# Kernel optimization log

Measured on AMD Instinct MI355X. Metric: run time of the kernel, lower is better.

The kernel has to match this reference:

```python
import jax, jax.numpy as jnp
import numpy as np

EMBED_DIM = 1024
NUM_HEADS = 16
HEAD_DIM = EMBED_DIM // NUM_HEADS
B, T_Q, T_K = 2, 2048, 2048


def setup_inputs() -> dict:
    key = jax.random.key(0)
    ks = jax.random.split(key, 11)
    s = 1.0 / np.sqrt(EMBED_DIM)
    return {
        "query": jax.random.normal(ks[0], (B, T_Q, EMBED_DIM), jnp.float32),
        "key": jax.random.normal(ks[1], (B, T_K, EMBED_DIM), jnp.float32),
        "value": jax.random.normal(ks[2], (B, T_K, EMBED_DIM), jnp.float32),
        "Wq": jax.random.normal(ks[3], (EMBED_DIM, EMBED_DIM), jnp.float32) * s,
        "bq": jnp.zeros((EMBED_DIM,), jnp.float32),
        "Wk": jax.random.normal(ks[4], (EMBED_DIM, EMBED_DIM), jnp.float32) * s,
        "bk": jnp.zeros((EMBED_DIM,), jnp.float32),
        "Wv": jax.random.normal(ks[5], (EMBED_DIM, EMBED_DIM), jnp.float32) * s,
        "bv": jnp.zeros((EMBED_DIM,), jnp.float32),
        "Wo": jax.random.normal(ks[6], (EMBED_DIM, EMBED_DIM), jnp.float32) * s,
        "bo": jnp.zeros((EMBED_DIM,), jnp.float32),
    }


def reference(query, key, value, Wq, bq, Wk, bk, Wv, bv, Wo, bo):
    b, tq, _ = query.shape
    tk = key.shape[1]
    # projections -> [B, H, T, Dh]
    q = (query @ Wq.T + bq).reshape(b, tq, NUM_HEADS, HEAD_DIM).transpose(0, 2, 1, 3)
    k = (key @ Wk.T + bk).reshape(b, tk, NUM_HEADS, HEAD_DIM).transpose(0, 2, 1, 3)
    v = (value @ Wv.T + bv).reshape(b, tk, NUM_HEADS, HEAD_DIM).transpose(0, 2, 1, 3)
    scores = jnp.einsum("bhqd,bhkd->bhqk", q, k) / np.sqrt(HEAD_DIM)
    attn = jax.nn.softmax(scores, axis=-1)
    attn = jnp.nan_to_num(attn, nan=0.0)  # matches torch.nan_to_num; dropout is eval-mode identity
    out = jnp.einsum("bhqk,bhkd->bhqd", attn, v)
    out = out.transpose(0, 2, 1, 3).reshape(b, tq, EMBED_DIM)
    return out @ Wo.T + bo
```

## Files before the change

### kernel.cpp

```cpp
#include <hip/hip_runtime.h>
#include <hip/hip_bf16.h>
#include <cmath>


typedef short bf16x8 __attribute__((ext_vector_type(8)));
typedef short bf16x4 __attribute__((ext_vector_type(4)));
typedef float f32x4 __attribute__((ext_vector_type(4)));

#define B_ 2
#define T_ 2048
#define E_ 1024
#define H_ 16
#define DH_ 64
#define M_ 4096
#define QSCALE 0.1803368801111204f

static __device__ __forceinline__ short f2bf(float f) {
    __hip_bfloat16 h = __float2bfloat16(f);
    return *reinterpret_cast<short*>(&h);
}

static __device__ __forceinline__ float bf2f(short s) {
    unsigned u = ((unsigned)(unsigned short)s) << 16;
    float f;
    __builtin_memcpy(&f, &u, 4);
    return f;
}

static __device__ __forceinline__ short f2bf_r(float f) {
    unsigned u;
    __builtin_memcpy(&u, &f, 4);
    return (short)((u + 0x8000u) >> 16);
}

static __device__ __forceinline__ float fast_exp2(float x) {
#if __has_builtin(__builtin_amdgcn_exp2f)
    return __builtin_amdgcn_exp2f(x);
#else
    float y;
    asm volatile("v_exp_f32 %0, %1" : "=v"(y) : "v"(x));
    return y;
#endif
}

static __device__ __forceinline__ bf16x8 cvt8(const float4 a, const float4 b) {
    bf16x8 r;
    r[0] = f2bf(a.x); r[1] = f2bf(a.y); r[2] = f2bf(a.z); r[3] = f2bf(a.w);
    r[4] = f2bf(b.x); r[5] = f2bf(b.y); r[6] = f2bf(b.z); r[7] = f2bf(b.w);
    return r;
}

static __device__ __forceinline__ void async_copy16(const short* g, short* l) {
    __builtin_amdgcn_global_load_lds(
        (const __attribute__((address_space(1))) unsigned int*)g,
        (__attribute__((address_space(3))) unsigned int*)l, 16, 0, 0);
}

__global__ __launch_bounds__(256) void conv_bf16(
    const float* __restrict__ q, const float* __restrict__ k, const float* __restrict__ v,
    const float* __restrict__ wq, const float* __restrict__ wk,
    const float* __restrict__ wv, const float* __restrict__ wo,
    short* __restrict__ qo, short* __restrict__ ko, short* __restrict__ vo,
    short* __restrict__ wqo, short* __restrict__ wko,
    short* __restrict__ wvo, short* __restrict__ woo) {
    const int y = blockIdx.y;
    const float* src; short* dst; int n;
    switch (y) {
        case 0: src = q;  dst = qo;  n = M_ * E_; break;
        case 1: src = k;  dst = ko;  n = M_ * E_; break;
        case 2: src = v;  dst = vo;  n = M_ * E_; break;
        case 3: src = wq; dst = wqo; n = E_ * E_; break;
        case 4: src = wk; dst = wko; n = E_ * E_; break;
        case 5: src = wv; dst = wvo; n = E_ * E_; break;
        default: src = wo; dst = woo; n = E_ * E_; break;
    }
    const int idx = (blockIdx.x * 256 + threadIdx.x) * 8;
    if (idx >= n) return;
    const float4* p = (const float4*)(src + idx);
    *(bf16x8*)(dst + idx) = cvt8(p[0], p[1]);
}

template <int CMODE>
__device__ __forceinline__ void gemm128_tile(const short* __restrict__ A,
                                             const short* __restrict__ W,
                                             const float* __restrict__ bias,
                                             void* __restrict__ C, int bx, int by,
                                             float scale) {
    __shared__ short Asm[128 * 64];
    __shared__ short Wsm[128 * 64];
    const int tid = threadIdx.x;
    const int wave = tid >> 6, lane = tid & 63, quad = lane >> 4, l16 = lane & 15;
    const int wr = wave >> 1, wc = wave & 1;
    const int m_base = by * 128, n_base = bx * 128;
    const int xk = l16 & 7;
    const int srowA = (lane >> 3), scc = lane & 7;

    f32x4 acc[4][4] = {};

    for (int k0 = 0; k0 < E_; k0 += 64) {
#pragma unroll
        for (int i = 0; i < 4; i++) {
            const int row = i * 32 + wave * 8 + srowA;
            const int gc = (scc ^ (row & 7)) * 8;
            async_copy16(&A[(size_t)(m_base + row) * E_ + k0 + gc],
                         &Asm[(i * 256 + wave * 64) * 8]);
            async_copy16(&W[(size_t)(n_base + row) * E_ + k0 + gc],
                         &Wsm[(i * 256 + wave * 64) * 8]);
        }
        __syncthreads();

#pragma unroll
        for (int ks = 0; ks < 2; ks++) {
            bf16x8 af[4], wf[4];
#pragma unroll
            for (int i = 0; i < 4; i++) {
                const int rw = wr * 64 + i * 16 + l16;
                af[i] = *(const bf16x8*)&Asm[rw * 64 + (((ks * 4 + quad) ^ xk) * 8)];
            }
#pragma unroll
            for (int j = 0; j < 4; j++) {
                const int rw = wc * 64 + j * 16 + l16;
                wf[j] = *(const bf16x8*)&Wsm[rw * 64 + (((ks * 4 + quad) ^ xk) * 8)];
            }
#pragma unroll
            for (int i = 0; i < 4; i++)
#pragma unroll
                for (int j = 0; j < 4; j++)
                    acc[i][j] = __builtin_amdgcn_mfma_f32_16x16x32_bf16(af[i], wf[j], acc[i][j], 0, 0, 0);
        }
        __syncthreads();
    }

    if (CMODE == 2) {
#pragma unroll
        for (int j = 0; j < 4; j++) {
            const int col = n_base + wc * 64 + j * 16 + l16;
            const float bval = bias[col];
            const int h = col >> 6, d = col & 63;
#pragma unroll
            for (int i = 0; i < 4; i++) {
                const int m0 = m_base + wr * 64 + i * 16 + quad * 4;
                const int b = m0 >> 11, t0 = m0 & 2047;
                bf16x4 v;
#pragma unroll
                for (int r = 0; r < 4; r++) v[r] = f2bf(acc[i][j][r] + bval);
                *(bf16x4*)&((short*)C)[((size_t)(b * H_ + h) * DH_ + d) * T_ + t0] = v;
            }
        }
    } else {
#pragma unroll
        for (int j = 0; j < 4; j++) {
            const int col = n_base + wc * 64 + j * 16 + l16;
            const float bval = bias[col];
#pragma unroll
            for (int i = 0; i < 4; i++)
#pragma unroll
                for (int r = 0; r < 4; r++) {
                    const int m = m_base + wr * 64 + i * 16 + quad * 4 + r;
                    ((short*)C)[(size_t)m * E_ + col] = f2bf((acc[i][j][r] + bval) * scale);
                }
        }
    }
}

__global__ __launch_bounds__(256) void qkv_gemm_fast(
    const short* __restrict__ q, const short* __restrict__ k, const short* __restrict__ v,
    const short* __restrict__ Wq, const short* __restrict__ Wk, const short* __restrict__ Wv,
    const float* __restrict__ bq, const float* __restrict__ bk, const float* __restrict__ bv,
    short* __restrict__ Qb, short* __restrict__ Kb, short* __restrict__ Vtb) {
    const int z = blockIdx.z;
    if (z == 0)      gemm128_tile<0>(q, Wq, bq, Qb,  blockIdx.x, blockIdx.y, QSCALE);
    else if (z == 1) gemm128_tile<0>(k, Wk, bk, Kb,  blockIdx.x, blockIdx.y, 1.0f);
    else             gemm128_tile<2>(v, Wv, bv, Vtb, blockIdx.x, blockIdx.y, 1.0f);
}

__global__ __launch_bounds__(256) void o_gemm_fast(const short* __restrict__ A,
                                                   const short* __restrict__ W,
                                                   const float* __restrict__ bias,
                                                   float* __restrict__ C) {
    __shared__ short Asm[128 * 64];
    __shared__ short Wsm[64 * 64];
    const int tid = threadIdx.x;
    const int wave = tid >> 6, lane = tid & 63, quad = lane >> 4, l16 = lane & 15;
    const int m_base = blockIdx.y * 128, n_base = blockIdx.x * 64;
    const int xk = l16 & 7;
    const int srowA = (lane >> 3), scc = lane & 7;

    f32x4 acc[2][4] = {};

    for (int k0 = 0; k0 < E_; k0 += 64) {
#pragma unroll
        for (int i = 0; i < 4; i++) {
            const int row = i * 32 + wave * 8 + srowA;
            const int gc = (scc ^ (row & 7)) * 8;
            async_copy16(&A[(size_t)(m_base + row) * E_ + k0 + gc],
                         &Asm[(i * 256 + wave * 64) * 8]);
        }
#pragma unroll
        for (int i = 0; i < 2; i++) {
            const int row = i * 32 + wave * 8 + srowA;
            const int gc = (scc ^ (row & 7)) * 8;
            async_copy16(&W[(size_t)(n_base + row) * E_ + k0 + gc],
                         &Wsm[(i * 256 + wave * 64) * 8]);
        }
        __syncthreads();

#pragma unroll
        for (int ks = 0; ks < 2; ks++) {
            bf16x8 af[2], wf[4];
#pragma unroll
            for (int i = 0; i < 2; i++) {
                const int rw = wave * 32 + i * 16 + l16;
                af[i] = *(const bf16x8*)&Asm[rw * 64 + (((ks * 4 + quad) ^ xk) * 8)];
            }
#pragma unroll
            for (int j = 0; j < 4; j++) {
                const int rw = j * 16 + l16;
                wf[j] = *(const bf16x8*)&Wsm[rw * 64 + (((ks * 4 + quad) ^ xk) * 8)];
            }
#pragma unroll
            for (int i = 0; i < 2; i++)
#pragma unroll
                for (int j = 0; j < 4; j++)
                    acc[i][j] = __builtin_amdgcn_mfma_f32_16x16x32_bf16(af[i], wf[j], acc[i][j], 0, 0, 0);
        }
        __syncthreads();
    }

#pragma unroll
    for (int j = 0; j < 4; j++) {
        const int col = n_base + j * 16 + l16;
        const float bval = bias[col];
#pragma unroll
        for (int i = 0; i < 2; i++)
#pragma unroll
            for (int r = 0; r < 4; r++) {
                const int m = m_base + wave * 32 + i * 16 + quad * 4 + r;
                C[(size_t)m * E_ + col] = acc[i][j][r] + bval;
            }
    }
}

__global__ __launch_bounds__(256) void attn_split(const short* __restrict__ Qb,
                                                  const short* __restrict__ Kb,
                                                  const short* __restrict__ Vtb,
                                                  short* __restrict__ Op,
                                                  float* __restrict__ Ls) {
    __shared__ short Kl[2][64][68];
    __shared__ short Vl[2][64][68];
    __shared__ short Pl[4][32][68];

    const int tid = threadIdx.x;
    const int wave = tid >> 6, lane = tid & 63, quad = lane >> 4, l16 = lane & 15;
    const int bh = blockIdx.x;
    const int b = bh >> 4, h = bh & 15;
    const int ksp = blockIdx.z;
    const int q0 = blockIdx.y * 128 + wave * 32;
    const int kt0 = ksp * (T_ / 2);
    const size_t base = ((size_t)b * T_) * E_ + (size_t)h * DH_;
    const size_t vbase = (size_t)bh * DH_ * T_;
    short* Opk = Op + (size_t)ksp * M_ * E_;
    float* Lsk = Ls + (size_t)ksp * 32 * T_ + (size_t)bh * T_;

    bf16x8 qf[2][2];
#pragma unroll
    for (int rt = 0; rt < 2; rt++)
#pragma unroll
        for (int ks = 0; ks < 2; ks++)
            qf[rt][ks] = *(const bf16x8*)&Qb[base + (size_t)(q0 + rt * 16 + l16) * E_ + ks * 32 + quad * 8];

    bf16x8 ones;
#pragma unroll
    for (int j = 0; j < 8; j++) ones[j] = (short)0x3F80;

    f32x4 oacc[2][4] = {};
    f32x4 lacc[2] = {};

    const int srow = tid >> 2;
    const int sc = (tid & 3) * 16;

    {
        const size_t krow = base + (size_t)(kt0 + srow) * E_;
        *(bf16x8*)&Kl[0][srow][sc]     = *(const bf16x8*)&Kb[krow + sc];
        *(bf16x8*)&Kl[0][srow][sc + 8] = *(const bf16x8*)&Kb[krow + sc + 8];
        const size_t vrow = vbase + (size_t)srow * T_ + kt0;
        *(bf16x8*)&Vl[0][srow][sc]     = *(const bf16x8*)&Vtb[vrow + sc];
        *(bf16x8*)&Vl[0][srow][sc + 8] = *(const bf16x8*)&Vtb[vrow + sc + 8];
    }
    __syncthreads();

    for (int it = 0; it < T_ / 128; it++) {
        const int cur = it & 1;
        const bool have = (it + 1) < T_ / 128;

        bf16x8 nk0, nk1, nv0, nv1;
        if (have) {
            const int kt = kt0 + (it + 1) * 64;
            const size_t krow = base + (size_t)(kt + srow) * E_;
            nk0 = *(const bf16x8*)&Kb[krow + sc];
            nk1 = *(const bf16x8*)&Kb[krow + sc + 8];
            const size_t vrow = vbase + (size_t)srow * T_ + kt;
            nv0 = *(const bf16x8*)&Vtb[vrow + sc];
            nv1 = *(const bf16x8*)&Vtb[vrow + sc + 8];
        }

        f32x4 sacc[2][4] = {};
#pragma unroll
        for (int ks = 0; ks < 2; ks++) {
            bf16x8 kf[4];
#pragma unroll
            for (int kn = 0; kn < 4; kn++)
                kf[kn] = *(const bf16x8*)&Kl[cur][kn * 16 + l16][ks * 32 + quad * 8];
#pragma unroll
            for (int rt = 0; rt < 2; rt++)
#pragma unroll
                for (int kn = 0; kn < 4; kn++)
                    sacc[rt][kn] = __builtin_amdgcn_mfma_f32_16x16x32_bf16(qf[rt][ks], kf[kn], sacc[rt][kn], 0, 0, 0);
        }

#pragma unroll
        for (int rt = 0; rt < 2; rt++)
#pragma unroll
            for (int r = 0; r < 4; r++) {
                short* prow = &Pl[wave][rt * 16 + quad * 4 + r][0];
                prow[l16]      = f2bf_r(fast_exp2(sacc[rt][0][r]));
                prow[16 + l16] = f2bf_r(fast_exp2(sacc[rt][1][r]));
                prow[32 + l16] = f2bf_r(fast_exp2(sacc[rt][2][r]));
                prow[48 + l16] = f2bf_r(fast_exp2(sacc[rt][3][r]));
            }
        asm volatile("s_waitcnt lgkmcnt(0)" ::: "memory");

#pragma unroll
        for (int ks = 0; ks < 2; ks++) {
            bf16x8 pf[2];
#pragma unroll
            for (int rt = 0; rt < 2; rt++)
                pf[rt] = *(const bf16x8*)&Pl[wave][rt * 16 + l16][ks * 32 + quad * 8];
#pragma unroll
            for (int rt = 0; rt < 2; rt++)
                lacc[rt] = __builtin_amdgcn_mfma_f32_16x16x32_bf16(pf[rt], ones, lacc[rt], 0, 0, 0);
#pragma unroll
            for (int dn = 0; dn < 4; dn++) {
                bf16x8 vf = *(const bf16x8*)&Vl[cur][dn * 16 + l16][ks * 32 + quad * 8];
#pragma unroll
                for (int rt = 0; rt < 2; rt++)
                    oacc[rt][dn] = __builtin_amdgcn_mfma_f32_16x16x32_bf16(pf[rt], vf, oacc[rt][dn], 0, 0, 0);
            }
        }

        if (have) {
            *(bf16x8*)&Kl[cur ^ 1][srow][sc]     = nk0;
            *(bf16x8*)&Kl[cur ^ 1][srow][sc + 8] = nk1;
            *(bf16x8*)&Vl[cur ^ 1][srow][sc]     = nv0;
            *(bf16x8*)&Vl[cur ^ 1][srow][sc + 8] = nv1;
        }
        __syncthreads();
    }

#pragma unroll
    for (int rt = 0; rt < 2; rt++) {
#pragma unroll
        for (int dn = 0; dn < 4; dn++)
#pragma unroll
            for (int r = 0; r < 4; r++)
                Opk[base + (size_t)(q0 + rt * 16 + quad * 4 + r) * E_ + dn * 16 + l16] =
                    f2bf(oacc[rt][dn][r]);
        if (l16 == 0) {
#pragma unroll
            for (int r = 0; r < 4; r++)
                Lsk[q0 + rt * 16 + quad * 4 + r] = lacc[rt][r];
        }
    }
}

__global__ __launch_bounds__(256) void combine(const short* __restrict__ Op,
                                               const float* __restrict__ Ls,
                                               short* __restrict__ Qb) {
    const int idx = (blockIdx.x * 256 + threadIdx.x) * 8;
    const int row = idx >> 10;
    const int e = idx & 1023;
    const int h = e >> 6;
    const int b = row >> 11, t = row & 2047;
    const size_t lidx = ((size_t)(b * H_ + h)) * T_ + t;
    const float l = Ls[lidx] + Ls[(size_t)32 * T_ + lidx];
    const float inv = 1.0f / l;
    bf16x8 a = *(const bf16x8*)&Op[idx];
    bf16x8 c = *(const bf16x8*)&Op[(size_t)M_ * E_ + idx];
    bf16x8 o;
#pragma unroll
    for (int j = 0; j < 8; j++) o[j] = f2bf((bf2f(a[j]) + bf2f(c[j])) * inv);
    *(bf16x8*)&Qb[idx] = o;
}

__global__ __launch_bounds__(256) void attn(short* __restrict__ QO,
                                            const short* __restrict__ Kb,
                                            const short* __restrict__ Vtb) {
    __shared__ short Kl[2][64][68];
    __shared__ short Vl[2][64][68];
    __shared__ short Pl[4][32][68];

    const int tid = threadIdx.x;
    const int wave = tid >> 6, lane = tid & 63, quad = lane >> 4, l16 = lane & 15;
    const int bh = blockIdx.x;
    const int b = bh >> 4, h = bh & 15;
    const int q0 = blockIdx.y * 128 + wave * 32;
    const size_t base = ((size_t)b * T_) * E_ + (size_t)h * DH_;
    const size_t vbase = (size_t)bh * DH_ * T_;

    bf16x8 qf[2][2];
#pragma unroll
    for (int rt = 0; rt < 2; rt++)
#pragma unroll
        for (int ks = 0; ks < 2; ks++)
            qf[rt][ks] = *(const bf16x8*)&QO[base + (size_t)(q0 + rt * 16 + l16) * E_ + ks * 32 + quad * 8];

    bf16x8 ones;
#pragma unroll
    for (int j = 0; j < 8; j++) ones[j] = (short)0x3F80;

    f32x4 oacc[2][4] = {};
    f32x4 lacc[2] = {};

    const int srow = tid >> 2;
    const int sc = (tid & 3) * 16;

    {
        const size_t krow = base + (size_t)srow * E_;
        *(bf16x8*)&Kl[0][srow][sc]     = *(const bf16x8*)&Kb[krow + sc];
        *(bf16x8*)&Kl[0][srow][sc + 8] = *(const bf16x8*)&Kb[krow + sc + 8];
        const size_t vrow = vbase + (size_t)srow * T_;
        *(bf16x8*)&Vl[0][srow][sc]     = *(const bf16x8*)&Vtb[vrow + sc];
        *(bf16x8*)&Vl[0][srow][sc + 8] = *(const bf16x8*)&Vtb[vrow + sc + 8];
    }
    __syncthreads();

    for (int it = 0; it < T_ / 64; it++) {
        const int cur = it & 1;
        const bool have = (it + 1) < T_ / 64;

        bf16x8 nk0, nk1, nv0, nv1;
        if (have) {
            const int kt = (it + 1) * 64;
            const size_t krow = base + (size_t)(kt + srow) * E_;
            nk0 = *(const bf16x8*)&Kb[krow + sc];
            nk1 = *(const bf16x8*)&Kb[krow + sc + 8];
            const size_t vrow = vbase + (size_t)srow * T_ + kt;
            nv0 = *(const bf16x8*)&Vtb[vrow + sc];
            nv1 = *(const bf16x8*)&Vtb[vrow + sc + 8];
        }

        f32x4 sacc[2][4] = {};
#pragma unroll
        for (int ks = 0; ks < 2; ks++) {
            bf16x8 kf[4];
#pragma unroll
            for (int kn = 0; kn < 4; kn++)
                kf[kn] = *(const bf16x8*)&Kl[cur][kn * 16 + l16][ks * 32 + quad * 8];
#pragma unroll
            for (int rt = 0; rt < 2; rt++)
#pragma unroll
                for (int kn = 0; kn < 4; kn++)
                    sacc[rt][kn] = __builtin_amdgcn_mfma_f32_16x16x32_bf16(qf[rt][ks], kf[kn], sacc[rt][kn], 0, 0, 0);
        }

#pragma unroll
        for (int rt = 0; rt < 2; rt++)
#pragma unroll
            for (int r = 0; r < 4; r++) {
                short* prow = &Pl[wave][rt * 16 + quad * 4 + r][0];
                prow[l16]      = f2bf_r(fast_exp2(sacc[rt][0][r]));
                prow[16 + l16] = f2bf_r(fast_exp2(sacc[rt][1][r]));
                prow[32 + l16] = f2bf_r(fast_exp2(sacc[rt][2][r]));
                prow[48 + l16] = f2bf_r(fast_exp2(sacc[rt][3][r]));
            }
        asm volatile("s_waitcnt lgkmcnt(0)" ::: "memory");

#pragma unroll
        for (int ks = 0; ks < 2; ks++) {
            bf16x8 pf[2];
#pragma unroll
            for (int rt = 0; rt < 2; rt++)
                pf[rt] = *(const bf16x8*)&Pl[wave][rt * 16 + l16][ks * 32 + quad * 8];
#pragma unroll
            for (int rt = 0; rt < 2; rt++)
                lacc[rt] = __builtin_amdgcn_mfma_f32_16x16x32_bf16(pf[rt], ones, lacc[rt], 0, 0, 0);
#pragma unroll
            for (int dn = 0; dn < 4; dn++) {
                bf16x8 vf = *(const bf16x8*)&Vl[cur][dn * 16 + l16][ks * 32 + quad * 8];
#pragma unroll
                for (int rt = 0; rt < 2; rt++)
                    oacc[rt][dn] = __builtin_amdgcn_mfma_f32_16x16x32_bf16(pf[rt], vf, oacc[rt][dn], 0, 0, 0);
            }
        }

        if (have) {
            *(bf16x8*)&Kl[cur ^ 1][srow][sc]     = nk0;
            *(bf16x8*)&Kl[cur ^ 1][srow][sc + 8] = nk1;
            *(bf16x8*)&Vl[cur ^ 1][srow][sc]     = nv0;
            *(bf16x8*)&Vl[cur ^ 1][srow][sc + 8] = nv1;
        }
        __syncthreads();
    }

    float inv[2][4];
#pragma unroll
    for (int rt = 0; rt < 2; rt++)
#pragma unroll
        for (int r = 0; r < 4; r++) inv[rt][r] = 1.0f / lacc[rt][r];

#pragma unroll
    for (int rt = 0; rt < 2; rt++)
#pragma unroll
        for (int dn = 0; dn < 4; dn++)
#pragma unroll
            for (int r = 0; r < 4; r++) {
                const float v = oacc[rt][dn][r] * inv[rt][r];
                QO[base + (size_t)(q0 + rt * 16 + quad * 4 + r) * E_ + dn * 16 + l16] = f2bf(v);
            }
}

template <int A_BF16, int CMODE>
__device__ __forceinline__ void gemm_tile(const void* __restrict__ A,
                                          const float* __restrict__ W,
                                          const float* __restrict__ bias,
                                          void* __restrict__ C, int bx, int by,
                                          float scale) {
    __shared__ short Alds[128][40];
    __shared__ short Wlds[128][40];
    const int tid = threadIdx.x;
    const int wave = tid >> 6, lane = tid & 63, quad = lane >> 4, l16 = lane & 15;
    const int wr = wave >> 1, wc = wave & 1;
    const int m_base = by * 128, n_base = bx * 128;
    const int srow = tid >> 1, sch = (tid & 1) * 16;

    f32x4 acc[4][4] = {};

    for (int k0 = 0; k0 < E_; k0 += 32) {
        bf16x8 av0, av1, wv0, wv1;
        if (A_BF16) {
            const short* Ab = (const short*)A;
            av0 = *(const bf16x8*)&Ab[(size_t)(m_base + srow) * E_ + k0 + sch];
            av1 = *(const bf16x8*)&Ab[(size_t)(m_base + srow) * E_ + k0 + sch + 8];
        } else {
            const float4* p = (const float4*)((const float*)A +
                              (size_t)(m_base + srow) * E_ + k0 + sch);
            av0 = cvt8(p[0], p[1]);
            av1 = cvt8(p[2], p[3]);
        }
        {
            const float4* p = (const float4*)(W + (size_t)(n_base + srow) * E_ + k0 + sch);
            wv0 = cvt8(p[0], p[1]);
            wv1 = cvt8(p[2], p[3]);
        }
        *(bf16x8*)&Alds[srow][sch]     = av0;
        *(bf16x8*)&Alds[srow][sch + 8] = av1;
        *(bf16x8*)&Wlds[srow][sch]     = wv0;
        *(bf16x8*)&Wlds[srow][sch + 8] = wv1;
        __syncthreads();

        bf16x8 af[4], bfv[4];
#pragma unroll
        for (int i = 0; i < 4; i++)
            af[i] = *(const bf16x8*)&Alds[wr * 64 + i * 16 + l16][quad * 8];
#pragma unroll
        for (int j = 0; j < 4; j++)
            bfv[j] = *(const bf16x8*)&Wlds[wc * 64 + j * 16 + l16][quad * 8];
#pragma unroll
        for (int i = 0; i < 4; i++)
#pragma unroll
            for (int j = 0; j < 4; j++)
                acc[i][j] = __builtin_amdgcn_mfma_f32_16x16x32_bf16(af[i], bfv[j], acc[i][j], 0, 0, 0);
        __syncthreads();
    }

    if (CMODE == 2) {
#pragma unroll
        for (int j = 0; j < 4; j++) {
            const int col = n_base + wc * 64 + j * 16 + l16;
            const float bval = bias[col];
            const int h = col >> 6, d = col & 63;
#pragma unroll
            for (int i = 0; i < 4; i++) {
                const int m0 = m_base + wr * 64 + i * 16 + quad * 4;
                const int b = m0 >> 11, t0 = m0 & 2047;
                bf16x4 v;
#pragma unroll
                for (int r = 0; r < 4; r++) v[r] = f2bf(acc[i][j][r] + bval);
                *(bf16x4*)&((short*)C)[((size_t)(b * H_ + h) * DH_ + d) * T_ + t0] = v;
            }
        }
    } else {
#pragma unroll
        for (int j = 0; j < 4; j++) {
            const int col = n_base + wc * 64 + j * 16 + l16;
            const float bval = bias[col];
#pragma unroll
            for (int i = 0; i < 4; i++)
#pragma unroll
                for (int r = 0; r < 4; r++) {
                    const int m = m_base + wr * 64 + i * 16 + quad * 4 + r;
                    const float v = (acc[i][j][r] + bval) * scale;
                    if (CMODE == 1) ((float*)C)[(size_t)m * E_ + col] = v;
                    else            ((short*)C)[(size_t)m * E_ + col] = f2bf(v);
                }
        }
    }
}

__global__ __launch_bounds__(256) void qkv_gemm_slow(
    const float* __restrict__ q, const float* __restrict__ k, const float* __restrict__ v,
    const float* __restrict__ Wq, const float* __restrict__ Wk, const float* __restrict__ Wv,
    const float* __restrict__ bq, const float* __restrict__ bk, const float* __restrict__ bv,
    short* __restrict__ Qb, short* __restrict__ Kb, short* __restrict__ Vtb) {
    const int z = blockIdx.z;
    if (z == 0)      gemm_tile<0, 0>(q, Wq, bq, Qb,  blockIdx.x, blockIdx.y, QSCALE);
    else if (z == 1) gemm_tile<0, 0>(k, Wk, bk, Kb,  blockIdx.x, blockIdx.y, 1.0f);
    else             gemm_tile<0, 2>(v, Wv, bv, Vtb, blockIdx.x, blockIdx.y, 1.0f);
}

__global__ __launch_bounds__(256) void o_gemm_slow(const short* __restrict__ A,
                                                   const float* __restrict__ W,
                                                   const float* __restrict__ bias,
                                                   float* __restrict__ C) {
    gemm_tile<1, 1>(A, W, bias, C, blockIdx.x, blockIdx.y, 1.0f);
}

extern "C" void kernel_launch(void* const* d_in, const int* in_sizes, int n_in,
                              void* d_out, int out_size, void* d_ws, size_t ws_size,
                              hipStream_t stream) {
    const float* query = (const float*)d_in[0];
    const float* key   = (const float*)d_in[1];
    const float* value = (const float*)d_in[2];
    const float* Wq = (const float*)d_in[3];
    const float* bq = (const float*)d_in[4];
    const float* Wk = (const float*)d_in[5];
    const float* bk = (const float*)d_in[6];
    const float* Wv = (const float*)d_in[7];
    const float* bv = (const float*)d_in[8];
    const float* Wo = (const float*)d_in[9];
    const float* bo = (const float*)d_in[10];

    const size_t NE = (size_t)M_ * E_;
    const size_t WE = (size_t)E_ * E_;

    short* Qb  = (short*)d_ws;
    short* Vtb = Qb + NE;
    short* Kb  = (short*)d_out;

    dim3 blk(256);
    const bool fast = ws_size >= (size_t)48 * 1024 * 1024;

    if (fast) {
        short* Qin = Vtb + NE;
        short* Kin = Qin + NE;
        short* Vin = Kin + NE;
        short* Wqb = Vin + NE;
        short* Wkb = Wqb + WE;
        short* Wvb = Wkb + WE;
        short* Wob = Wvb + WE;

        conv_bf16<<<dim3(2048, 7), blk, 0, stream>>>(query, key, value, Wq, Wk, Wv, Wo,
                                                     Qin, Kin, Vin, Wqb, Wkb, Wvb, Wob);
        qkv_gemm_fast<<<dim3(8, 32, 3), blk, 0, stream>>>(Qin, Kin, Vin,
                                                          Wqb, Wkb, Wvb, bq, bk, bv,
                                                          Qb, Kb, Vtb);
        attn_split<<<dim3(B_ * H_, T_ / 128, 2), blk, 0, stream>>>(
            Qb, Kb, Vtb, Qin, (float*)Vin);
        combine<<<dim3((M_ * E_) / (256 * 8)), blk, 0, stream>>>(
            Qin, (const float*)Vin, Qb);
        o_gemm_fast<<<dim3(16, 32), blk, 0, stream>>>(Qb, Wob, bo, (float*)d_out);
    } else {
        qkv_gemm_slow<<<dim3(8, 32, 3), blk, 0, stream>>>(query, key, value,
                                                          Wq, Wk, Wv, bq, bk, bv,
                                                          Qb, Kb, Vtb);
        attn<<<dim3(B_ * H_, T_ / 128), blk, 0, stream>>>(Qb, Kb, Vtb);
        o_gemm_slow<<<dim3(8, 32), blk, 0, stream>>>(Qb, Wo, bo, (float*)d_out);
    }
}
```

Baseline: 245.4 us.

## Enlarge attention query tile, use async swizzled K/V loads, stage V-transpose stores

Result: faster. 235.4 us (-4.0%).

```diff
diff --git a/kernel.cpp b/kernel.cpp
--- a/kernel.cpp
+++ b/kernel.cpp
@@ -86,8 +86,9 @@
                                              const float* __restrict__ bias,
                                              void* __restrict__ C, int bx, int by,
                                              float scale) {
-    __shared__ short Asm[128 * 64];
-    __shared__ short Wsm[128 * 64];
+    __shared__ short SMEM[128 * 132];
+    short* Asm = SMEM;
+    short* Wsm = SMEM + 128 * 64;
     const int tid = threadIdx.x;
     const int wave = tid >> 6, lane = tid & 63, quad = lane >> 4, l16 = lane & 15;
     const int wr = wave >> 1, wc = wave & 1;
@@ -134,18 +135,27 @@
     if (CMODE == 2) {
 #pragma unroll
         for (int j = 0; j < 4; j++) {
-            const int col = n_base + wc * 64 + j * 16 + l16;
-            const float bval = bias[col];
-            const int h = col >> 6, d = col & 63;
+            const int drow = wc * 64 + j * 16 + l16;
+            const float bval = bias[n_base + drow];
 #pragma unroll
             for (int i = 0; i < 4; i++) {
-                const int m0 = m_base + wr * 64 + i * 16 + quad * 4;
-                const int b = m0 >> 11, t0 = m0 & 2047;
+                const int tcol = wr * 64 + i * 16 + quad * 4;
                 bf16x4 v;
 #pragma unroll
                 for (int r = 0; r < 4; r++) v[r] = f2bf(acc[i][j][r] + bval);
-                *(bf16x4*)&((short*)C)[((size_t)(b * H_ + h) * DH_ + d) * T_ + t0] = v;
-            }
+                *(bf16x4*)&SMEM[drow * 132 + tcol] = v;
+            }
+        }
+        __syncthreads();
+        const int bb = m_base >> 11, t0 = m_base & 2047;
+#pragma unroll
+        for (int u0 = 0; u0 < 8; u0++) {
+            const int u = u0 * 256 + tid;
+            const int row = u >> 4, ch = u & 15;
+            const int col = n_base + row;
+            const int hh = col >> 6, dd = col & 63;
+            bf16x8 val = *(const bf16x8*)&SMEM[row * 132 + ch * 8];
+            *(bf16x8*)&((short*)C)[((size_t)(bb * H_ + hh) * DH_ + dd) * T_ + t0 + ch * 8] = val;
         }
     } else {
 #pragma unroll
@@ -241,13 +251,13 @@
     }
 }
 
-__global__ __launch_bounds__(256) void attn_split(const short* __restrict__ Qb,
-                                                  const short* __restrict__ Kb,
-                                                  const short* __restrict__ Vtb,
-                                                  short* __restrict__ Op,
-                                                  float* __restrict__ Ls) {
-    __shared__ short Kl[2][64][68];
-    __shared__ short Vl[2][64][68];
+__global__ __launch_bounds__(256, 2) void attn_split(const short* __restrict__ Qb,
+                                                     const short* __restrict__ Kb,
+                                                     const short* __restrict__ Vtb,
+                                                     short* __restrict__ Op,
+                                                     float* __restrict__ Ls) {
+    __shared__ short Kl[2][64 * 64];
+    __shared__ short Vl[2][64 * 64];
     __shared__ short Pl[4][32][68];
 
     const int tid = threadIdx.x;
@@ -255,16 +265,16 @@
     const int bh = blockIdx.x;
     const int b = bh >> 4, h = bh & 15;
     const int ksp = blockIdx.z;
-    const int q0 = blockIdx.y * 128 + wave * 32;
+    const int q0 = blockIdx.y * 256 + wave * 64;
     const int kt0 = ksp * (T_ / 2);
     const size_t base = ((size_t)b * T_) * E_ + (size_t)h * DH_;
     const size_t vbase = (size_t)bh * DH_ * T_;
     short* Opk = Op + (size_t)ksp * M_ * E_;
     float* Lsk = Ls + (size_t)ksp * 32 * T_ + (size_t)bh * T_;
 
-    bf16x8 qf[2][2];
-#pragma unroll
-    for (int rt = 0; rt < 2; rt++)
+    bf16x8 qf[4][2];
+#pragma unroll
+    for (int rt = 0; rt < 4; rt++)
 #pragma unroll
         for (int ks = 0; ks < 2; ks++)
             qf[rt][ks] = *(const bf16x8*)&Qb[base + (size_t)(q0 + rt * 16 + l16) * E_ + ks * 32 + quad * 8];
@@ -273,103 +283,102 @@
 #pragma unroll
     for (int j = 0; j < 8; j++) ones[j] = (short)0x3F80;
 
-    f32x4 oacc[2][4] = {};
-    f32x4 lacc[2] = {};
-
-    const int srow = tid >> 2;
-    const int sc = (tid & 3) * 16;
-
-    {
-        const size_t krow = base + (size_t)(kt0 + srow) * E_;
-        *(bf16x8*)&Kl[0][srow][sc]     = *(const bf16x8*)&Kb[krow + sc];
-        *(bf16x8*)&Kl[0][srow][sc + 8] = *(const bf16x8*)&Kb[krow + sc + 8];
-        const size_t vrow = vbase + (size_t)srow * T_ + kt0;
-        *(bf16x8*)&Vl[0][srow][sc]     = *(const bf16x8*)&Vtb[vrow + sc];
-        *(bf16x8*)&Vl[0][srow][sc + 8] = *(const bf16x8*)&Vtb[vrow + sc + 8];
+    f32x4 oacc[4][4] = {};
+    f32x4 lacc[4] = {};
+
+    const int srow = wave * 8 + (lane >> 3);
+    const int scc = lane & 7;
+    const int xk = l16 & 7;
+
+#pragma unroll
+    for (int i = 0; i < 2; i++) {
+        const int row = i * 32 + srow;
+        const int gc = (scc ^ (row & 7)) * 8;
+        async_copy16(&Kb[base + (size_t)(kt0 + row) * E_ + gc], &Kl[0][(i * 256 + wave * 64) * 8]);
+        async_copy16(&Vtb[vbase + (size_t)row * T_ + kt0 + gc], &Vl[0][(i * 256 + wave * 64) * 8]);
     }
     __syncthreads();
 
-    for (int it = 0; it < T_ / 128; it++) {
+    for (int it = 0; it < (T_ / 2) / 64; it++) {
         const int cur = it & 1;
-        const bool have = (it + 1) < T_ / 128;
-
-        bf16x8 nk0, nk1, nv0, nv1;
-        if (have) {
+        if (it + 1 < (T_ / 2) / 64) {
             const int kt = kt0 + (it + 1) * 64;
-            const size_t krow = base + (size_t)(kt + srow) * E_;
-            nk0 = *(const bf16x8*)&Kb[krow + sc];
-            nk1 = *(const bf16x8*)&Kb[krow + sc + 8];
-            const size_t vrow = vbase + (size_t)srow * T_ + kt;
-            nv0 = *(const bf16x8*)&Vtb[vrow + sc];
-            nv1 = *(const bf16x8*)&Vtb[vrow + sc + 8];
-        }
-
-        f32x4 sacc[2][4] = {};
-#pragma unroll
-        for (int ks = 0; ks < 2; ks++) {
-            bf16x8 kf[4];
-#pragma unroll
-            for (int kn = 0; kn < 4; kn++)
-                kf[kn] = *(const bf16x8*)&Kl[cur][kn * 16 + l16][ks * 32 + quad * 8];
-#pragma unroll
-            for (int rt = 0; rt < 2; rt++)
+#pragma unroll
+            for (int i = 0; i < 2; i++) {
+                const int row = i * 32 + srow;
+                const int gc = (scc ^ (row & 7)) * 8;
+                async_copy16(&Kb[base + (size_t)(kt + row) * E_ + gc],
+                             &Kl[cur ^ 1][(i * 256 + wave * 64) * 8]);
+                async_copy16(&Vtb[vbase + (size_t)row * T_ + kt + gc],
+                             &Vl[cur ^ 1][(i * 256 + wave * 64) * 8]);
+            }
+        }
+
+#pragma unroll
+        for (int rp = 0; rp < 2; rp++) {
+            f32x4 sacc[2][4] = {};
+#pragma unroll
+            for (int ks = 0; ks < 2; ks++) {
+                bf16x8 kf[4];
 #pragma unroll
                 for (int kn = 0; kn < 4; kn++)
-                    sacc[rt][kn] = __builtin_amdgcn_mfma_f32_16x16x32_bf16(qf[rt][ks], kf[kn], sacc[rt][kn], 0, 0, 0);
-        }
-
-#pragma unroll
-        for (int rt = 0; rt < 2; rt++)
-#pragma unroll
-            for (int r = 0; r < 4; r++) {
-                short* prow = &Pl[wave][rt * 16 + quad * 4 + r][0];
-                prow[l16]      = f2bf_r(fast_exp2(sacc[rt][0][r]));
-                prow[16 + l16] = f2bf_r(fast_exp2(sacc[rt][1][r]));
-                prow[32 + l16] = f2bf_r(fast_exp2(sacc[rt][2][r]));
-                prow[48 + l16] = f2bf_r(fast_exp2(sacc[rt][3][r]));
-            }
-        asm volatile("s_waitcnt lgkmcnt(0)" ::: "memory");
-
-#pragma unroll
-        for (int ks = 0; ks < 2; ks++) {
-            bf16x8 pf[2];
-#pragma unroll
-            for (int rt = 0; rt < 2; rt++)
-                pf[rt] = *(const bf16x8*)&Pl[wave][rt * 16 + l16][ks * 32 + quad * 8];
-#pragma unroll
-            for (int rt = 0; rt < 2; rt++)
-                lacc[rt] = __builtin_amdgcn_mfma_f32_16x16x32_bf16(pf[rt], ones, lacc[rt], 0, 0, 0);
-#pragma unroll
-            for (int dn = 0; dn < 4; dn++) {
-                bf16x8 vf = *(const bf16x8*)&Vl[cur][dn * 16 + l16][ks * 32 + quad * 8];
-#pragma unroll
-                for (int rt = 0; rt < 2; rt++)
-                    oacc[rt][dn] = __builtin_amdgcn_mfma_f32_16x16x32_bf16(pf[rt], vf, oacc[rt][dn], 0, 0, 0);
-            }
-        }
-
-        if (have) {
-            *(bf16x8*)&Kl[cur ^ 1][srow][sc]     = nk0;
-            *(bf16x8*)&Kl[cur ^ 1][srow][sc + 8] = nk1;
-            *(bf16x8*)&Vl[cur ^ 1][srow][sc]     = nv0;
-            *(bf16x8*)&Vl[cur ^ 1][srow][sc + 8] = nv1;
-        }
-        __syncthreads();
-    }
-
-#pragma unroll
-    for (int rt = 0; rt < 2; rt++) {
+                    kf[kn] = *(const bf16x8*)&Kl[cur][(kn * 16 + l16) * 64 + (((ks * 4 + quad) ^ xk) * 8)];
+#pragma unroll
+                for (int r2 = 0; r2 < 2; r2++)
+#pragma unroll
+                    for (int kn = 0; kn < 4; kn++)
+                        sacc[r2][kn] = __builtin_amdgcn_mfma_f32_16x16x32_bf16(
+                            qf[rp * 2 + r2][ks], kf[kn], sacc[r2][kn], 0, 0, 0);
+            }
+
+#pragma unroll
+            for (int r2 = 0; r2 < 2; r2++)
+#pragma unroll
+                for (int r = 0; r < 4; r++) {
+                    short* prow = &Pl[wave][r2 * 16 + quad * 4 + r][0];
+                    prow[l16]      = f2bf_r(fast_exp2(sacc[r2][0][r]));
+                    prow[16 + l16] = f2bf_r(fast_exp2(sacc[r2][1][r]));
+                    prow[32 + l16] = f2bf_r(fast_exp2(sacc[r2][2][r]));
+                    prow[48 + l16] = f2bf_r(fast_exp2(sacc[r2][3][r]));
+                }
+            asm volatile("s_waitcnt lgkmcnt(0)" ::: "memory");
+
+#pragma unroll
+            for (int ks = 0; ks < 2; ks++) {
+                bf16x8 pf[2];
+#pragma unroll
+                for (int r2 = 0; r2 < 2; r2++)
+                    pf[r2] = *(const bf16x8*)&Pl[wave][r2 * 16 + l16][ks * 32 + quad * 8];
+#pragma unroll
+                for (int r2 = 0; r2 < 2; r2++)
+                    lacc[rp * 2 + r2] = __builtin_amdgcn_mfma_f32_16x16x32_bf16(
+                        pf[r2], ones, lacc[rp * 2 + r2], 0, 0, 0);
+#pragma unroll
+                for (int dn = 0; dn < 4; dn++) {
+                    bf16x8 vf = *(const bf16x8*)&Vl[cur][(dn * 16 + l16) * 64 + (((ks * 4 + quad) ^ xk) * 8)];
+#pragma unroll
+                    for (int r2 = 0; r2 < 2; r2++)
+                        oacc[rp * 2 + r2][dn] = __builtin_amdgcn_mfma_f32_16x16x32_bf16(
+                            pf[r2], vf, oacc[rp * 2 + r2][dn], 0, 0, 0);
+                }
+            }
+            asm volatile("s_waitcnt lgkmcnt(0)" ::: "memory");
+        }
+        __syncthreads();
+    }
+
+#pragma unroll
+    for (int rt = 0; rt < 4; rt++) {
 #pragma unroll
         for (int dn = 0; dn < 4; dn++)
 #pragma unroll
             for (int r = 0; r < 4; r++)
                 Opk[base + (size_t)(q0 + rt * 16 + quad * 4 + r) * E_ + dn * 16 + l16] =
                     f2bf(oacc[rt][dn][r]);
-        if (l16 == 0) {
+        if (l16 == 0)
 #pragma unroll
             for (int r = 0; r < 4; r++)
                 Lsk[q0 + rt * 16 + quad * 4 + r] = lacc[rt][r];
-        }
     }
 }
 
@@ -664,7 +673,7 @@
         qkv_gemm_fast<<<dim3(8, 32, 3), blk, 0, stream>>>(Qin, Kin, Vin,
                                                           Wqb, Wkb, Wvb, bq, bk, bv,
                                                           Qb, Kb, Vtb);
-        attn_split<<<dim3(B_ * H_, T_ / 128, 2), blk, 0, stream>>>(
+        attn_split<<<dim3(B_ * H_, T_ / 256, 2), blk, 0, stream>>>(
             Qb, Kb, Vtb, Qin, (float*)Vin);
         combine<<<dim3((M_ * E_) / (256 * 8)), blk, 0, stream>>>(
             Qin, (const float*)Vin, Qb);
```
